# Kernel optimization log

Measured on AMD Instinct MI355X. Metric: run time of the kernel, lower is better.

## Reference

```python
import jax, jax.numpy as jnp
import numpy as np

B, L, H, D, M = 4, 2048, 16, 64, 128
EPS = 1e-6


def _create_projection_matrix(key, m, d):
    nb_full_blocks = m // d
    keys = jax.random.split(key, nb_full_blocks + 2)
    blocks = []
    for i in range(nb_full_blocks):
        unstructured = jax.random.normal(keys[i], (d, d), dtype=jnp.float32)
        q, _ = jnp.linalg.qr(unstructured)
        blocks.append(q.T)
    remaining = m - nb_full_blocks * d
    if remaining > 0:
        unstructured = jax.random.normal(keys[nb_full_blocks], (d, d), dtype=jnp.float32)
        q, _ = jnp.linalg.qr(unstructured)
        blocks.append(q.T[:remaining])
    final = jnp.concatenate(blocks, axis=0)  # [m, d]
    multiplier = jnp.linalg.norm(jax.random.normal(keys[-1], (m, d), dtype=jnp.float32), axis=1)
    return multiplier[:, None] * final


def setup_inputs() -> dict:
    key = jax.random.key(0)
    kq, kk, kv, kp = jax.random.split(key, 4)
    return {
        "q": jax.random.normal(kq, (B, L, H, D), dtype=jnp.float32),
        "k": jax.random.normal(kk, (B, L, H, D), dtype=jnp.float32),
        "v": jax.random.normal(kv, (B, L, H, D), dtype=jnp.float32),
        "projection_matrix": _create_projection_matrix(kp, M, D),
    }


def _softmax_kernel(data, proj, is_query, eps=EPS):
    # data: [B,L,H,D], proj: [M,D]
    data = (data.shape[-1] ** -0.25) * data
    ratio = proj.shape[0] ** -0.5
    data_dash = jnp.einsum('blhd,md->blhm', data, proj)  # [B,L,H,M]
    diag = jnp.sum(data * data, axis=-1, keepdims=True) * 0.5  # [B,L,H,1]
    if is_query:
        mx = jnp.max(data_dash, axis=-1, keepdims=True)
    else:
        mx = jnp.max(data_dash, axis=(1, 3), keepdims=True)
    return ratio * (jnp.exp(data_dash - diag - mx) + eps)


def reference(q, k, v, projection_matrix):
    qp = _softmax_kernel(q, projection_matrix, True)   # [B,L,H,M]
    kp = _softmax_kernel(k, projection_matrix, False)  # [B,L,H,M]
    # move L to the front for the causal scan
    qs = jnp.swapaxes(qp, 0, 1)  # [L,B,H,M]
    ks = jnp.swapaxes(kp, 0, 1)  # [L,B,H,M]
    vs = jnp.swapaxes(v, 0, 1)   # [L,B,H,D]

    def step(carry, inp):
        s, dsum = carry                 # s: [B,H,M,D], dsum: [B,H,M]
        q_t, k_t, v_t = inp
        s = s + k_t[..., :, None] * v_t[..., None, :]  # outer product accumulate
        dsum = dsum + k_t
        num = jnp.einsum('bhmd,bhm->bhd', s, q_t)      # [B,H,D]
        den = jnp.einsum('bhm,bhm->bh', q_t, dsum)     # [B,H]
        return (s, dsum), (num, den)

    init = (jnp.zeros((qs.shape[1], qs.shape[2], qs.shape[3], vs.shape[3]), qs.dtype),
            jnp.zeros_like(ks[0]))
    _, (nums, dens) = jax.lax.scan(step, init, (qs, ks, vs))
    av = jnp.swapaxes(nums, 0, 1)          # [B,L,H,D]
    norm = jnp.swapaxes(dens, 0, 1)[..., None]  # [B,L,H,1]
    return av / norm
```

## Files before the change

### kernel.cpp

```cpp
#include <hip/hip_runtime.h>
#include <math.h>

#define B_ 4
#define L_ 2048
#define H_ 16
#define D_ 64
#define M_ 128
#define TC_ 64
#define NC_ (L_ / TC_)
#define EPSK 1e-6f
#define DATA_SCALE 0.35355339059327379f
#define RATIO 0.08838834764831845f

typedef __bf16 bf16;
typedef bf16 bf16x4 __attribute__((ext_vector_type(4)));
typedef bf16 bf16x8 __attribute__((ext_vector_type(8)));
typedef float floatx4 __attribute__((ext_vector_type(4)));

#define PK128 136
#define PK64 72

__device__ __forceinline__ unsigned pk(bf16 a, bf16 b) {
    return (unsigned)__builtin_bit_cast(unsigned short, a) |
           ((unsigned)__builtin_bit_cast(unsigned short, b) << 16);
}

__device__ __forceinline__ unsigned enc_f(float f) {
    unsigned u = __float_as_uint(f);
    return (u & 0x80000000u) ? ~u : (u | 0x80000000u);
}
__device__ __forceinline__ float dec_f(unsigned u) {
    unsigned b = (u & 0x80000000u) ? (u ^ 0x80000000u) : ~u;
    return __uint_as_float(b);
}

__global__ __launch_bounds__(256) void proj_split(const float* __restrict__ proj,
                                                  bf16* __restrict__ pfh,
                                                  bf16* __restrict__ pfl,
                                                  unsigned* __restrict__ mx) {
    int f = blockIdx.x * 256 + threadIdx.x;
    if (blockIdx.x == 0 && threadIdx.x < B_ * H_) mx[threadIdx.x] = 0u;
    int tc = f >> 7, k0h = (f >> 6) & 1, lane = f & 63;
    int lr = lane & 15, quad = lane >> 4;
    const float* src = proj + (16 * tc + lr) * 64 + k0h * 32 + quad * 8;
    float4 x0 = *(const float4*)src;
    float4 x1 = *(const float4*)(src + 4);
    float a[8] = {x0.x, x0.y, x0.z, x0.w, x1.x, x1.y, x1.z, x1.w};
    bf16x8 hi, lo;
#pragma unroll
    for (int e = 0; e < 8; e++) {
        bf16 h = (bf16)a[e];
        hi[e] = h;
        lo[e] = (bf16)(a[e] - (float)h);
    }
    *(bf16x8*)(pfh + (size_t)f * 8) = hi;
    *(bf16x8*)(pfl + (size_t)f * 8) = lo;
}

template <int MODE>
__device__ __forceinline__ void feat_body(const float* __restrict__ data,
                                          const bf16* __restrict__ pfh,
                                          const bf16* __restrict__ pfl,
                                          unsigned* __restrict__ mxk,
                                          bf16* __restrict__ outp,
                                          bf16* __restrict__ outT,
                                          int blk, bf16* sc, float* wred) {
    int tid = threadIdx.x;
    int c = blk & 31, h = (blk >> 5) & 15, b = blk >> 9;
    int l0 = c * 64;
    int w = tid >> 6, lane = tid & 63, lr = lane & 15, quad = lane >> 4;

    const float* drow = data +
        ((size_t)(b * L_ + l0 + 16 * w + lr) * H_ + h) * D_ + quad * 8;
    bf16x8 ah[2], al[2];
    float ss = 0.f;
#pragma unroll
    for (int k0 = 0; k0 < 2; k0++) {
        float4 x0 = *(const float4*)(drow + k0 * 32);
        float4 x1 = *(const float4*)(drow + k0 * 32 + 4);
        float a[8] = {x0.x, x0.y, x0.z, x0.w, x1.x, x1.y, x1.z, x1.w};
#pragma unroll
        for (int e = 0; e < 8; e++) {
            float s = DATA_SCALE * a[e];
            if (MODE != 0) ss += s * s;
            bf16 hh = (bf16)s;
            ah[k0][e] = hh;
            if (MODE != 0) al[k0][e] = (bf16)(s - (float)hh);
        }
    }
    float ssrow = 0.f;
    if (MODE != 0) {
        ss += __shfl_xor(ss, 16, 64);
        ss += __shfl_xor(ss, 32, 64);
        ssrow = 0.5f * ss;
    }

    floatx4 acc[8];
#pragma unroll
    for (int tc = 0; tc < 8; tc++) acc[tc] = (floatx4){0.f, 0.f, 0.f, 0.f};

    const bf16x8* ph = (const bf16x8*)pfh + lane;
    const bf16x8* pl = (const bf16x8*)pfl + lane;
#pragma unroll
    for (int tc = 0; tc < 8; tc++) {
#pragma unroll
        for (int k0 = 0; k0 < 2; k0++) {
            bf16x8 bh = ph[(tc * 2 + k0) * 64];
            acc[tc] = __builtin_amdgcn_mfma_f32_16x16x32_bf16(ah[k0], bh, acc[tc], 0, 0, 0);
            if (MODE != 0) {
                bf16x8 bl = pl[(tc * 2 + k0) * 64];
                acc[tc] = __builtin_amdgcn_mfma_f32_16x16x32_bf16(al[k0], bh, acc[tc], 0, 0, 0);
                acc[tc] = __builtin_amdgcn_mfma_f32_16x16x32_bf16(ah[k0], bl, acc[tc], 0, 0, 0);
            }
        }
    }

    if (MODE == 0) {
        float mm = acc[0][0];
#pragma unroll
        for (int tc = 0; tc < 8; tc++)
#pragma unroll
            for (int reg = 0; reg < 4; reg++) mm = fmaxf(mm, acc[tc][reg]);
#pragma unroll
        for (int off = 1; off < 64; off <<= 1) mm = fmaxf(mm, __shfl_xor(mm, off, 64));
        if (lane == 0) wred[w] = mm;
        __syncthreads();
        if (tid == 0) {
            float g = fmaxf(fmaxf(wred[0], wred[1]), fmaxf(wred[2], wred[3]));
            atomicMax(&mxk[b * H_ + h], enc_f(g));
        }
        return;
    }

    int t0 = 16 * w + 4 * quad;
    float mxg = 0.f;
    if (MODE == 1) mxg = dec_f(mxk[b * H_ + h]);

    float rm[4];
    if (MODE == 2) {
#pragma unroll
        for (int reg = 0; reg < 4; reg++) {
            float m = acc[0][reg];
#pragma unroll
            for (int tc = 1; tc < 8; tc++) m = fmaxf(m, acc[tc][reg]);
            m = fmaxf(m, __shfl_xor(m, 1, 64));
            m = fmaxf(m, __shfl_xor(m, 2, 64));
            m = fmaxf(m, __shfl_xor(m, 4, 64));
            m = fmaxf(m, __shfl_xor(m, 8, 64));
            rm[reg] = m;
        }
    }

#pragma unroll
    for (int reg = 0; reg < 4; reg++) {
        float dg = __shfl(ssrow, 4 * quad + reg, 64);
        float sh = (MODE == 1) ? (dg + mxg) : (dg + rm[reg]);
#pragma unroll
        for (int tc = 0; tc < 8; tc++) {
            float val = RATIO * (__expf(acc[tc][reg] - sh) + EPSK);
            sc[(t0 + reg) * 130 + 16 * tc + lr] = (bf16)val;
        }
    }
    __syncthreads();

#pragma unroll
    for (int i = 0; i < 16; i++) {
        int e = tid + 256 * i;
        int row = e >> 6, mp = e & 63;
        unsigned u = pk(sc[row * 130 + 2 * mp], sc[row * 130 + 2 * mp + 1]);
        *(unsigned*)(outp + ((size_t)(b * L_ + l0 + row) * H_ + h) * M_ + 2 * mp) = u;
    }
    if (MODE == 1) {
#pragma unroll
        for (int i = 0; i < 16; i++) {
            int e = tid + 256 * i;
            int m = e >> 5, t2 = (e & 31) * 2;
            unsigned u = pk(sc[t2 * 130 + m], sc[(t2 + 1) * 130 + m]);
            *(unsigned*)(outT + ((size_t)(b * H_ + h) * M_ + m) * L_ + l0 + t2) = u;
        }
    }
}

__device__ __forceinline__ void vtr_body(const float* __restrict__ v,
                                         bf16* __restrict__ vbT,
                                         int blk, bf16* vt) {
    int tid = threadIdx.x;
    int c = blk & 31, hh = (blk >> 5) & 15, b = blk >> 9;
#pragma unroll
    for (int i = 0; i < 4; i++) {
        int ch = tid + 256 * i;
        int row = ch >> 4, c4 = ch & 15;
        size_t gb = ((size_t)(b * L_ + c * 64 + row) * H_ + hh) * D_;
        float4 x = *(const float4*)(v + gb + c4 * 4);
        unsigned* lp = (unsigned*)(vt + row * 66 + c4 * 4);
        lp[0] = pk((bf16)x.x, (bf16)x.y);
        lp[1] = pk((bf16)x.z, (bf16)x.w);
    }
    __syncthreads();
    size_t ob = (size_t)((b * H_ + hh) * D_) * (size_t)L_ + c * 64;
#pragma unroll
    for (int i = 0; i < 8; i++) {
        int e2 = tid + 256 * i;
        int d = e2 >> 5, tau2 = (e2 & 31) * 2;
        *(unsigned*)(vbT + ob + (size_t)d * L_ + tau2) =
            pk(vt[tau2 * 66 + d], vt[(tau2 + 1) * 66 + d]);
    }
}

__global__ __launch_bounds__(256) void pre3(const float* __restrict__ q,
                                            const float* __restrict__ k,
                                            const float* __restrict__ v,
                                            const bf16* __restrict__ pfh,
                                            const bf16* __restrict__ pfl,
                                            unsigned* __restrict__ mxk,
                                            bf16* __restrict__ qp,
                                            bf16* __restrict__ vbT) {
    __shared__ __align__(16) bf16 arena[64 * 130];
    __shared__ float wred[4];
    int blk = blockIdx.x;
    if (blk < 2048) {
        feat_body<2>(q, pfh, pfl, mxk, qp, (bf16*)nullptr, blk, arena, wred);
    } else if (blk < 4096) {
        feat_body<0>(k, pfh, pfl, mxk, (bf16*)nullptr, (bf16*)nullptr, blk - 2048,
                     arena, wred);
    } else {
        vtr_body(v, vbT, blk - 4096, arena);
    }
}

__global__ __launch_bounds__(256) void feat_k(const float* __restrict__ k,
                                              const bf16* __restrict__ pfh,
                                              const bf16* __restrict__ pfl,
                                              unsigned* __restrict__ mxk,
                                              bf16* __restrict__ kp,
                                              bf16* __restrict__ kpT) {
    __shared__ __align__(16) bf16 arena[64 * 130];
    __shared__ float wred[4];
    feat_body<1>(k, pfh, pfl, mxk, kp, kpT, blockIdx.x, arena, wred);
}

__global__ __launch_bounds__(256) void chunk_mfma(const bf16* __restrict__ kpT,
                                                  const bf16* __restrict__ vbT,
                                                  bf16* __restrict__ S,
                                                  float* __restrict__ ds) {
    __shared__ __align__(16) bf16 kT[128 * PK64];
    __shared__ __align__(16) bf16 vT[64 * PK64];
    int tid = threadIdx.x;
    int blk = blockIdx.x;
    int c = blk & 31, bh = blk >> 5;
    int l0 = c * 64;
#pragma unroll
    for (int i = 0; i < 4; i++) {
        int ch = tid + 256 * i;
        int m = ch >> 3, c8 = ch & 7;
        *(uint4*)(kT + m * PK64 + c8 * 8) =
            ((const uint4*)kpT)[(((size_t)bh * M_ + m) * L_ + l0) / 8 + c8];
    }
#pragma unroll
    for (int i = 0; i < 2; i++) {
        int ch = tid + 256 * i;
        int d = ch >> 3, c8 = ch & 7;
        *(uint4*)(vT + d * PK64 + c8 * 8) =
            ((const uint4*)vbT)[(((size_t)bh * D_ + d) * L_ + l0) / 8 + c8];
    }
    __syncthreads();

    int w = tid >> 6, lane = tid & 63, lr = lane & 15, quad = lane >> 4;
    floatx4 acc[8];
#pragma unroll
    for (int tc = 0; tc < 8; tc++) acc[tc] = (floatx4){0.f, 0.f, 0.f, 0.f};
#pragma unroll
    for (int k0 = 0; k0 < 64; k0 += 32) {
        bf16x8 a = *(const bf16x8*)(vT + (16 * w + lr) * PK64 + k0 + quad * 8);
#pragma unroll
        for (int tc = 0; tc < 8; tc++) {
            bf16x8 bb = *(const bf16x8*)(kT + (16 * tc + lr) * PK64 + k0 + quad * 8);
            acc[tc] = __builtin_amdgcn_mfma_f32_16x16x32_bf16(a, bb, acc[tc], 0, 0, 0);
        }
    }

    float dsv = 0.f;
    {
        int m = tid >> 1, half = tid & 1;
        const bf16x8* kr = (const bf16x8*)(kT + m * PK64 + half * 32);
#pragma unroll
        for (int j = 0; j < 4; j++) {
            bf16x8 vv = kr[j];
#pragma unroll
            for (int e = 0; e < 8; e++) dsv += (float)vv[e];
        }
        dsv += __shfl_xor(dsv, 1, 64);
    }
    __syncthreads();

    bf16* scr = kT;
    int d0 = 16 * w + 4 * quad;
#pragma unroll
    for (int tc = 0; tc < 8; tc++)
#pragma unroll
        for (int reg = 0; reg < 4; reg++)
            scr[(d0 + reg) * 128 + 16 * tc + lr] = (bf16)acc[tc][reg];
    if ((tid & 1) == 0) ds[(size_t)blk * M_ + (tid >> 1)] = dsv;
    __syncthreads();
#pragma unroll
    for (int i = 0; i < 4; i++) {
        int e = tid + 256 * i;
        ((uint4*)S)[(size_t)blk * 1024 + e] = ((const uint4*)scr)[e];
    }
}

__global__ void prefix_SD(unsigned* __restrict__ S, float* __restrict__ ds) {
    int blk = blockIdx.x;
    int seg = blk & 15, bh = blk >> 4;
    int p = seg * 256 + threadIdx.x;
    size_t base = (size_t)bh * NC_ * 4096 + p;
    unsigned uv[NC_];
#pragma unroll
    for (int c = 0; c < NC_; c++) uv[c] = S[base + (size_t)c * 4096];
    float c0 = 0.f, c1 = 0.f;
#pragma unroll
    for (int c = 0; c < NC_; c++) {
        unsigned u = uv[c];
        float f0 = (float)__builtin_bit_cast(bf16, (unsigned short)(u & 0xffffu));
        float f1 = (float)__builtin_bit_cast(bf16, (unsigned short)(u >> 16));
        S[base + (size_t)c * 4096] = pk((bf16)c0, (bf16)c1);
        c0 += f0; c1 += f1;
    }
    if (seg == 0 && threadIdx.x < 128) {
        int m = threadIdx.x;
        size_t dbase = (size_t)bh * NC_ * M_ + m;
        float dv[NC_];
#pragma unroll
        for (int c = 0; c < NC_; c++) dv[c] = ds[dbase + (size_t)c * M_];
        float carry = 0.f;
#pragma unroll
        for (int c = 0; c < NC_; c++) {
            ds[dbase + (size_t)c * M_] = carry;
            carry += dv[c];
        }
    }
}

__global__ __launch_bounds__(256, 4) void attn_mfma(const bf16* __restrict__ qp,
                                                    const bf16* __restrict__ kp,
                                                    const bf16* __restrict__ vbT,
                                                    const bf16* __restrict__ Sp,
                                                    const float* __restrict__ dp,
                                                    float* __restrict__ out) {
    __shared__ __align__(16) bf16 vT[64 * PK64];
    __shared__ __align__(16) bf16 sc[64 * PK64];
    __shared__ float dprevL[128];

    int tid = threadIdx.x;
    int blk = blockIdx.x;
    int c = blk & 31, bh = blk >> 5;
    int h = bh & 15, b = bh >> 4;
    int l0 = c * 64;
    int w = tid >> 6, lane = tid & 63, lr = lane & 15, quad = lane >> 4;

#pragma unroll
    for (int i = 0; i < 2; i++) {
        int ch = tid + 256 * i;
        int d = ch >> 3, c8 = ch & 7;
        *(uint4*)(vT + d * PK64 + c8 * 8) =
            ((const uint4*)vbT)[(((size_t)bh * D_ + d) * L_ + l0) / 8 + c8];
    }
    if (tid < 128) dprevL[tid] = dp[(size_t)blk * M_ + tid];

    bf16x8 af[4];
    {
        const bf16* qb = qp + ((size_t)(b * L_ + l0 + 16 * w + lr) * H_ + h) * M_ + quad * 8;
#pragma unroll
        for (int k = 0; k < 4; k++) af[k] = *(const bf16x8*)(qb + 32 * k);
    }
    __syncthreads();

    float den0v = 0.f;
#pragma unroll
    for (int k = 0; k < 4; k++)
#pragma unroll
        for (int e = 0; e < 8; e++)
            den0v += (float)af[k][e] * dprevL[quad * 8 + 32 * k + e];
    den0v += __shfl_xor(den0v, 16, 64);
    den0v += __shfl_xor(den0v, 32, 64);

    floatx4 acc[4];
#pragma unroll
    for (int tc = 0; tc < 4; tc++) acc[tc] = (floatx4){0.f, 0.f, 0.f, 0.f};

    {
        const bf16* spb = Sp + (size_t)blk * 8192;
#pragma unroll
        for (int ki = 0; ki < 4; ki++) {
#pragma unroll
            for (int tc = 0; tc < 4; tc++) {
                bf16x8 bb = *(const bf16x8*)(spb + (16 * tc + lr) * 128 + 32 * ki + quad * 8);
                acc[tc] = __builtin_amdgcn_mfma_f32_16x16x32_bf16(af[ki], bb, acc[tc], 0, 0, 0);
            }
        }
    }

    floatx4 acc2[4];
#pragma unroll
    for (int tc = 0; tc < 4; tc++) acc2[tc] = (floatx4){0.f, 0.f, 0.f, 0.f};
    {
        const bf16* kpb = kp + ((size_t)(b * L_ + l0) * H_ + h) * M_ + quad * 8;
#pragma unroll
        for (int ki = 0; ki < 4; ki++) {
            for (int tc = 0; tc <= w; tc++) {
                bf16x8 bb = *(const bf16x8*)(kpb + (size_t)(16 * tc + lr) * (H_ * M_) + 32 * ki);
                acc2[tc] = __builtin_amdgcn_mfma_f32_16x16x32_bf16(af[ki], bb, acc2[tc], 0, 0, 0);
            }
        }
    }

    int t0 = 16 * w + 4 * quad;
    float densc[4];
    {
        float dsum[4] = {0.f, 0.f, 0.f, 0.f};
#pragma unroll
        for (int tc = 0; tc < 4; tc++) {
#pragma unroll
            for (int reg = 0; reg < 4; reg++) {
                int tg = t0 + reg, tau = 16 * tc + lr;
                float vv = (tc <= w) ? acc2[tc][reg] : 0.f;
                if (tau > tg) vv = 0.f;
                dsum[reg] += vv;
                sc[tg * PK64 + tau] = (bf16)vv;
            }
        }
#pragma unroll
        for (int reg = 0; reg < 4; reg++) {
            float s = dsum[reg];
            s += __shfl_xor(s, 1, 64);
            s += __shfl_xor(s, 2, 64);
            s += __shfl_xor(s, 4, 64);
            s += __shfl_xor(s, 8, 64);
            densc[reg] = s;
        }
    }

    {
        int kmax = (w >= 2) ? 64 : 32;
        for (int k0 = 0; k0 < kmax; k0 += 32) {
            bf16x8 a = *(const bf16x8*)(sc + (16 * w + lr) * PK64 + k0 + quad * 8);
#pragma unroll
            for (int tc = 0; tc < 4; tc++) {
                bf16x8 bb = *(const bf16x8*)(vT + (16 * tc + lr) * PK64 + k0 + quad * 8);
                acc[tc] = __builtin_amdgcn_mfma_f32_16x16x32_bf16(a, bb, acc[tc], 0, 0, 0);
            }
        }
    }

    {
        float inv[4];
#pragma unroll
        for (int reg = 0; reg < 4; reg++) {
            float d0 = __shfl(den0v, 4 * quad + reg, 64);
            inv[reg] = 1.0f / (d0 + densc[reg]);
        }
#pragma unroll
        for (int tc = 0; tc < 4; tc++)
#pragma unroll
            for (int reg = 0; reg < 4; reg++)
                out[((size_t)(b * L_ + l0 + t0 + reg) * H_ + h) * D_ + 16 * tc + lr] =
                    acc[tc][reg] * inv[reg];
    }
}

extern "C" void kernel_launch(void* const* d_in, const int* in_sizes, int n_in,
                              void* d_out, int out_size, void* d_ws, size_t ws_size,
                              hipStream_t stream) {
    const float* q = (const float*)d_in[0];
    const float* k = (const float*)d_in[1];
    const float* v = (const float*)d_in[2];
    const float* proj = (const float*)d_in[3];
    float* out = (float*)d_out;
    char* W = (char*)d_ws;

    bf16* qp   = (bf16*)(W);
    bf16* kp   = (bf16*)(W + 33554432ull);
    bf16* kpT  = (bf16*)(W + 67108864ull);
    bf16* vbT  = (bf16*)(W + 100663296ull);
    bf16* S    = (bf16*)(W + 117440512ull);
    float* ds  = (float*)(W + 150994944ull);
    unsigned* mx = (unsigned*)(W + 152043520ull);
    bf16* pfh  = (bf16*)(W + 152043776ull);
    bf16* pfl  = (bf16*)(W + 152060160ull);

    hipLaunchKernelGGL(proj_split, dim3(4), dim3(256), 0, stream, proj, pfh, pfl, mx);
    hipLaunchKernelGGL(pre3, dim3(6144), dim3(256), 0, stream,
                       q, k, v, pfh, pfl, mx, qp, vbT);
    hipLaunchKernelGGL(feat_k, dim3(2048), dim3(256), 0, stream,
                       k, pfh, pfl, mx, kp, kpT);
    hipLaunchKernelGGL(chunk_mfma, dim3(2048), dim3(256), 0, stream, kpT, vbT, S, ds);
    hipLaunchKernelGGL(prefix_SD, dim3(1024), dim3(256), 0, stream, (unsigned*)S, ds);
    hipLaunchKernelGGL(attn_mfma, dim3(2048), dim3(256), 0, stream,
                       qp, kp, vbT, S, ds, out);
}
```

Baseline: 235.1 us.

## Fuse query feature map into attention kernel and drop transposed intermediates

Query features are now computed inside the attention kernel, so the bf16 qp buffer is never written or read back. The key max pass becomes its own kernel. Key features are stored chunk-contiguous and transposed in shared memory inside chunk_v, which replaces the separate kpT buffer. The V conversion and transpose also move into chunk_v. This cuts global memory traffic and the large workspace, but the attention kernel gets extra MFMA work, more registers and more shared memory, which may lower occupancy.

```diff
diff --git a/kernel.cpp b/kernel.cpp
--- a/kernel.cpp
+++ b/kernel.cpp
@@ -17,8 +17,8 @@
 typedef bf16 bf16x8 __attribute__((ext_vector_type(8)));
 typedef float floatx4 __attribute__((ext_vector_type(4)));
 
-#define PK128 136
 #define PK64 72
+#define FS_ 136
 
 __device__ __forceinline__ unsigned pk(bf16 a, bf16 b) {
     return (unsigned)__builtin_bit_cast(unsigned short, a) |
@@ -57,104 +57,111 @@
     *(bf16x8*)(pfl + (size_t)f * 8) = lo;
 }
 
-template <int MODE>
-__device__ __forceinline__ void feat_body(const float* __restrict__ data,
-                                          const bf16* __restrict__ pfh,
-                                          const bf16* __restrict__ pfl,
-                                          unsigned* __restrict__ mxk,
-                                          bf16* __restrict__ outp,
-                                          bf16* __restrict__ outT,
-                                          int blk, bf16* sc, float* wred) {
+__global__ __launch_bounds__(256) void feat_max(const float* __restrict__ k,
+                                                const bf16* __restrict__ pfh,
+                                                unsigned* __restrict__ mxk) {
+    __shared__ float wred[4];
     int tid = threadIdx.x;
+    int blk = blockIdx.x;
     int c = blk & 31, h = (blk >> 5) & 15, b = blk >> 9;
     int l0 = c * 64;
     int w = tid >> 6, lane = tid & 63, lr = lane & 15, quad = lane >> 4;
 
-    const float* drow = data +
+    const float* drow = k +
         ((size_t)(b * L_ + l0 + 16 * w + lr) * H_ + h) * D_ + quad * 8;
-    bf16x8 ah[2], al[2];
-    float ss = 0.f;
+    bf16x8 ah[2];
 #pragma unroll
     for (int k0 = 0; k0 < 2; k0++) {
         float4 x0 = *(const float4*)(drow + k0 * 32);
         float4 x1 = *(const float4*)(drow + k0 * 32 + 4);
         float a[8] = {x0.x, x0.y, x0.z, x0.w, x1.x, x1.y, x1.z, x1.w};
 #pragma unroll
-        for (int e = 0; e < 8; e++) {
-            float s = DATA_SCALE * a[e];
-            if (MODE != 0) ss += s * s;
-            bf16 hh = (bf16)s;
-            ah[k0][e] = hh;
-            if (MODE != 0) al[k0][e] = (bf16)(s - (float)hh);
-        }
-    }
-    float ssrow = 0.f;
-    if (MODE != 0) {
-        ss += __shfl_xor(ss, 16, 64);
-        ss += __shfl_xor(ss, 32, 64);
-        ssrow = 0.5f * ss;
+        for (int e = 0; e < 8; e++) ah[k0][e] = (bf16)(DATA_SCALE * a[e]);
     }
 
     floatx4 acc[8];
 #pragma unroll
     for (int tc = 0; tc < 8; tc++) acc[tc] = (floatx4){0.f, 0.f, 0.f, 0.f};
-
     const bf16x8* ph = (const bf16x8*)pfh + lane;
-    const bf16x8* pl = (const bf16x8*)pfl + lane;
-#pragma unroll
-    for (int tc = 0; tc < 8; tc++) {
+#pragma unroll
+    for (int tc = 0; tc < 8; tc++)
 #pragma unroll
         for (int k0 = 0; k0 < 2; k0++) {
             bf16x8 bh = ph[(tc * 2 + k0) * 64];
             acc[tc] = __builtin_amdgcn_mfma_f32_16x16x32_bf16(ah[k0], bh, acc[tc], 0, 0, 0);
-            if (MODE != 0) {
-                bf16x8 bl = pl[(tc * 2 + k0) * 64];
-                acc[tc] = __builtin_amdgcn_mfma_f32_16x16x32_bf16(al[k0], bh, acc[tc], 0, 0, 0);
-                acc[tc] = __builtin_amdgcn_mfma_f32_16x16x32_bf16(ah[k0], bl, acc[tc], 0, 0, 0);
-            }
-        }
-    }
-
-    if (MODE == 0) {
-        float mm = acc[0][0];
-#pragma unroll
-        for (int tc = 0; tc < 8; tc++)
-#pragma unroll
-            for (int reg = 0; reg < 4; reg++) mm = fmaxf(mm, acc[tc][reg]);
-#pragma unroll
-        for (int off = 1; off < 64; off <<= 1) mm = fmaxf(mm, __shfl_xor(mm, off, 64));
-        if (lane == 0) wred[w] = mm;
-        __syncthreads();
-        if (tid == 0) {
-            float g = fmaxf(fmaxf(wred[0], wred[1]), fmaxf(wred[2], wred[3]));
-            atomicMax(&mxk[b * H_ + h], enc_f(g));
-        }
-        return;
-    }
+        }
+
+    float mm = acc[0][0];
+#pragma unroll
+    for (int tc = 0; tc < 8; tc++)
+#pragma unroll
+        for (int reg = 0; reg < 4; reg++) mm = fmaxf(mm, acc[tc][reg]);
+#pragma unroll
+    for (int off = 1; off < 64; off <<= 1) mm = fmaxf(mm, __shfl_xor(mm, off, 64));
+    if (lane == 0) wred[w] = mm;
+    __syncthreads();
+    if (tid == 0) {
+        float g = fmaxf(fmaxf(wred[0], wred[1]), fmaxf(wred[2], wred[3]));
+        atomicMax(&mxk[b * H_ + h], enc_f(g));
+    }
+}
+
+__global__ __launch_bounds__(256) void feat_k(const float* __restrict__ kin,
+                                              const bf16* __restrict__ pfh,
+                                              const bf16* __restrict__ pfl,
+                                              const unsigned* __restrict__ mxk,
+                                              bf16* __restrict__ kp) {
+    __shared__ __align__(16) bf16 sc[64 * 130];
+    int tid = threadIdx.x;
+    int blk = blockIdx.x;
+    int c = blk & 31, h = (blk >> 5) & 15, b = blk >> 9;
+    int l0 = c * 64;
+    int w = tid >> 6, lane = tid & 63, lr = lane & 15, quad = lane >> 4;
+
+    const float* drow = kin +
+        ((size_t)(b * L_ + l0 + 16 * w + lr) * H_ + h) * D_ + quad * 8;
+    bf16x8 ah[2], al[2];
+    float ss = 0.f;
+#pragma unroll
+    for (int k0 = 0; k0 < 2; k0++) {
+        float4 x0 = *(const float4*)(drow + k0 * 32);
+        float4 x1 = *(const float4*)(drow + k0 * 32 + 4);
+        float a[8] = {x0.x, x0.y, x0.z, x0.w, x1.x, x1.y, x1.z, x1.w};
+#pragma unroll
+        for (int e = 0; e < 8; e++) {
+            float s = DATA_SCALE * a[e];
+            ss += s * s;
+            bf16 hh = (bf16)s;
+            ah[k0][e] = hh;
+            al[k0][e] = (bf16)(s - (float)hh);
+        }
+    }
+    ss += __shfl_xor(ss, 16, 64);
+    ss += __shfl_xor(ss, 32, 64);
+    float ssrow = 0.5f * ss;
+
+    floatx4 acc[8];
+#pragma unroll
+    for (int tc = 0; tc < 8; tc++) acc[tc] = (floatx4){0.f, 0.f, 0.f, 0.f};
+    const bf16x8* ph = (const bf16x8*)pfh + lane;
+    const bf16x8* pl = (const bf16x8*)pfl + lane;
+#pragma unroll
+    for (int tc = 0; tc < 8; tc++)
+#pragma unroll
+        for (int k0 = 0; k0 < 2; k0++) {
+            bf16x8 bh = ph[(tc * 2 + k0) * 64];
+            bf16x8 bl = pl[(tc * 2 + k0) * 64];
+            acc[tc] = __builtin_amdgcn_mfma_f32_16x16x32_bf16(ah[k0], bh, acc[tc], 0, 0, 0);
+            acc[tc] = __builtin_amdgcn_mfma_f32_16x16x32_bf16(al[k0], bh, acc[tc], 0, 0, 0);
+            acc[tc] = __builtin_amdgcn_mfma_f32_16x16x32_bf16(ah[k0], bl, acc[tc], 0, 0, 0);
+        }
 
     int t0 = 16 * w + 4 * quad;
-    float mxg = 0.f;
-    if (MODE == 1) mxg = dec_f(mxk[b * H_ + h]);
-
-    float rm[4];
-    if (MODE == 2) {
-#pragma unroll
-        for (int reg = 0; reg < 4; reg++) {
-            float m = acc[0][reg];
-#pragma unroll
-            for (int tc = 1; tc < 8; tc++) m = fmaxf(m, acc[tc][reg]);
-            m = fmaxf(m, __shfl_xor(m, 1, 64));
-            m = fmaxf(m, __shfl_xor(m, 2, 64));
-            m = fmaxf(m, __shfl_xor(m, 4, 64));
-            m = fmaxf(m, __shfl_xor(m, 8, 64));
-            rm[reg] = m;
-        }
-    }
-
+    float mxg = dec_f(mxk[b * H_ + h]);
 #pragma unroll
     for (int reg = 0; reg < 4; reg++) {
         float dg = __shfl(ssrow, 4 * quad + reg, 64);
-        float sh = (MODE == 1) ? (dg + mxg) : (dg + rm[reg]);
+        float sh = dg + mxg;
 #pragma unroll
         for (int tc = 0; tc < 8; tc++) {
             float val = RATIO * (__expf(acc[tc][reg] - sh) + EPSK);
@@ -163,109 +170,52 @@
     }
     __syncthreads();
 
+    bf16* kout = kp + (size_t)blk * 8192;
 #pragma unroll
     for (int i = 0; i < 16; i++) {
         int e = tid + 256 * i;
         int row = e >> 6, mp = e & 63;
-        unsigned u = pk(sc[row * 130 + 2 * mp], sc[row * 130 + 2 * mp + 1]);
-        *(unsigned*)(outp + ((size_t)(b * L_ + l0 + row) * H_ + h) * M_ + 2 * mp) = u;
-    }
-    if (MODE == 1) {
-#pragma unroll
-        for (int i = 0; i < 16; i++) {
-            int e = tid + 256 * i;
-            int m = e >> 5, t2 = (e & 31) * 2;
-            unsigned u = pk(sc[t2 * 130 + m], sc[(t2 + 1) * 130 + m]);
-            *(unsigned*)(outT + ((size_t)(b * H_ + h) * M_ + m) * L_ + l0 + t2) = u;
-        }
-    }
-}
-
-__device__ __forceinline__ void vtr_body(const float* __restrict__ v,
-                                         bf16* __restrict__ vbT,
-                                         int blk, bf16* vt) {
-    int tid = threadIdx.x;
-    int c = blk & 31, hh = (blk >> 5) & 15, b = blk >> 9;
-#pragma unroll
-    for (int i = 0; i < 4; i++) {
-        int ch = tid + 256 * i;
-        int row = ch >> 4, c4 = ch & 15;
-        size_t gb = ((size_t)(b * L_ + c * 64 + row) * H_ + hh) * D_;
-        float4 x = *(const float4*)(v + gb + c4 * 4);
-        unsigned* lp = (unsigned*)(vt + row * 66 + c4 * 4);
-        lp[0] = pk((bf16)x.x, (bf16)x.y);
-        lp[1] = pk((bf16)x.z, (bf16)x.w);
-    }
-    __syncthreads();
-    size_t ob = (size_t)((b * H_ + hh) * D_) * (size_t)L_ + c * 64;
-#pragma unroll
-    for (int i = 0; i < 8; i++) {
-        int e2 = tid + 256 * i;
-        int d = e2 >> 5, tau2 = (e2 & 31) * 2;
-        *(unsigned*)(vbT + ob + (size_t)d * L_ + tau2) =
-            pk(vt[tau2 * 66 + d], vt[(tau2 + 1) * 66 + d]);
-    }
-}
-
-__global__ __launch_bounds__(256) void pre3(const float* __restrict__ q,
-                                            const float* __restrict__ k,
-                                            const float* __restrict__ v,
-                                            const bf16* __restrict__ pfh,
-                                            const bf16* __restrict__ pfl,
-                                            unsigned* __restrict__ mxk,
-                                            bf16* __restrict__ qp,
-                                            bf16* __restrict__ vbT) {
-    __shared__ __align__(16) bf16 arena[64 * 130];
-    __shared__ float wred[4];
-    int blk = blockIdx.x;
-    if (blk < 2048) {
-        feat_body<2>(q, pfh, pfl, mxk, qp, (bf16*)nullptr, blk, arena, wred);
-    } else if (blk < 4096) {
-        feat_body<0>(k, pfh, pfl, mxk, (bf16*)nullptr, (bf16*)nullptr, blk - 2048,
-                     arena, wred);
-    } else {
-        vtr_body(v, vbT, blk - 4096, arena);
-    }
-}
-
-__global__ __launch_bounds__(256) void feat_k(const float* __restrict__ k,
-                                              const bf16* __restrict__ pfh,
-                                              const bf16* __restrict__ pfl,
-                                              unsigned* __restrict__ mxk,
-                                              bf16* __restrict__ kp,
-                                              bf16* __restrict__ kpT) {
-    __shared__ __align__(16) bf16 arena[64 * 130];
-    __shared__ float wred[4];
-    feat_body<1>(k, pfh, pfl, mxk, kp, kpT, blockIdx.x, arena, wred);
-}
-
-__global__ __launch_bounds__(256) void chunk_mfma(const bf16* __restrict__ kpT,
-                                                  const bf16* __restrict__ vbT,
-                                                  bf16* __restrict__ S,
-                                                  float* __restrict__ ds) {
+        *(unsigned*)(kout + row * 128 + 2 * mp) =
+            pk(sc[row * 130 + 2 * mp], sc[row * 130 + 2 * mp + 1]);
+    }
+}
+
+__global__ __launch_bounds__(256) void chunk_v(const bf16* __restrict__ kp,
+                                               const float* __restrict__ v,
+                                               bf16* __restrict__ S,
+                                               float* __restrict__ ds,
+                                               bf16* __restrict__ vbT) {
     __shared__ __align__(16) bf16 kT[128 * PK64];
     __shared__ __align__(16) bf16 vT[64 * PK64];
     int tid = threadIdx.x;
     int blk = blockIdx.x;
     int c = blk & 31, bh = blk >> 5;
+    int h = bh & 15, b = bh >> 4;
     int l0 = c * 64;
+    int w = tid >> 6, lane = tid & 63, lr = lane & 15, quad = lane >> 4;
+
+    const bf16* kpt = kp + (size_t)blk * 8192;
 #pragma unroll
     for (int i = 0; i < 4; i++) {
-        int ch = tid + 256 * i;
-        int m = ch >> 3, c8 = ch & 7;
-        *(uint4*)(kT + m * PK64 + c8 * 8) =
-            ((const uint4*)kpT)[(((size_t)bh * M_ + m) * L_ + l0) / 8 + c8];
-    }
-#pragma unroll
-    for (int i = 0; i < 2; i++) {
-        int ch = tid + 256 * i;
-        int d = ch >> 3, c8 = ch & 7;
-        *(uint4*)(vT + d * PK64 + c8 * 8) =
-            ((const uint4*)vbT)[(((size_t)bh * D_ + d) * L_ + l0) / 8 + c8];
-    }
-    __syncthreads();
-
-    int w = tid >> 6, lane = tid & 63, lr = lane & 15, quad = lane >> 4;
+        int m8 = w * 4 + i;
+        bf16x8 kv = *(const bf16x8*)(kpt + lane * 128 + m8 * 8);
+#pragma unroll
+        for (int e = 0; e < 8; e++) kT[(m8 * 8 + e) * PK64 + lane] = kv[e];
+    }
+    {
+        const float* vrow = v + ((size_t)(b * L_ + l0 + lane) * H_ + h) * D_;
+#pragma unroll
+        for (int i = 0; i < 4; i++) {
+            int d4 = w * 4 + i;
+            float4 x = *(const float4*)(vrow + d4 * 4);
+            vT[(d4 * 4 + 0) * PK64 + lane] = (bf16)x.x;
+            vT[(d4 * 4 + 1) * PK64 + lane] = (bf16)x.y;
+            vT[(d4 * 4 + 2) * PK64 + lane] = (bf16)x.z;
+            vT[(d4 * 4 + 3) * PK64 + lane] = (bf16)x.w;
+        }
+    }
+    __syncthreads();
+
     floatx4 acc[8];
 #pragma unroll
     for (int tc = 0; tc < 8; tc++) acc[tc] = (floatx4){0.f, 0.f, 0.f, 0.f};
@@ -276,6 +226,17 @@
         for (int tc = 0; tc < 8; tc++) {
             bf16x8 bb = *(const bf16x8*)(kT + (16 * tc + lr) * PK64 + k0 + quad * 8);
             acc[tc] = __builtin_amdgcn_mfma_f32_16x16x32_bf16(a, bb, acc[tc], 0, 0, 0);
+        }
+    }
+
+    {
+        size_t ob = (size_t)(bh * D_) * (size_t)L_ + l0;
+#pragma unroll
+        for (int i = 0; i < 8; i++) {
+            int e2 = tid + 256 * i;
+            int d = e2 >> 5, tau2 = (e2 & 31) * 2;
+            *(unsigned*)(vbT + ob + (size_t)d * L_ + tau2) =
+                *(const unsigned*)(vT + d * PK64 + tau2);
         }
     }
 
@@ -341,15 +302,18 @@
     }
 }
 
-__global__ __launch_bounds__(256, 4) void attn_mfma(const bf16* __restrict__ qp,
-                                                    const bf16* __restrict__ kp,
-                                                    const bf16* __restrict__ vbT,
-                                                    const bf16* __restrict__ Sp,
-                                                    const float* __restrict__ dp,
-                                                    float* __restrict__ out) {
+__global__ __launch_bounds__(256, 4) void attn_q(const float* __restrict__ q,
+                                                 const bf16* __restrict__ pfh,
+                                                 const bf16* __restrict__ pfl,
+                                                 const bf16* __restrict__ kp,
+                                                 const bf16* __restrict__ vbT,
+                                                 const bf16* __restrict__ Sp,
+                                                 const float* __restrict__ dp,
+                                                 float* __restrict__ out) {
+    __shared__ __align__(16) bf16 fsc[64 * FS_];
     __shared__ __align__(16) bf16 vT[64 * PK64];
-    __shared__ __align__(16) bf16 sc[64 * PK64];
     __shared__ float dprevL[128];
+    bf16* sc = fsc;
 
     int tid = threadIdx.x;
     int blk = blockIdx.x;
@@ -367,13 +331,69 @@
     }
     if (tid < 128) dprevL[tid] = dp[(size_t)blk * M_ + tid];
 
+    const float* drow = q +
+        ((size_t)(b * L_ + l0 + 16 * w + lr) * H_ + h) * D_ + quad * 8;
+    bf16x8 ah[2], al[2];
+    float ss = 0.f;
+#pragma unroll
+    for (int k0 = 0; k0 < 2; k0++) {
+        float4 x0 = *(const float4*)(drow + k0 * 32);
+        float4 x1 = *(const float4*)(drow + k0 * 32 + 4);
+        float a[8] = {x0.x, x0.y, x0.z, x0.w, x1.x, x1.y, x1.z, x1.w};
+#pragma unroll
+        for (int e = 0; e < 8; e++) {
+            float s = DATA_SCALE * a[e];
+            ss += s * s;
+            bf16 hh = (bf16)s;
+            ah[k0][e] = hh;
+            al[k0][e] = (bf16)(s - (float)hh);
+        }
+    }
+    ss += __shfl_xor(ss, 16, 64);
+    ss += __shfl_xor(ss, 32, 64);
+    float ssrow = 0.5f * ss;
+
+    floatx4 facc[8];
+#pragma unroll
+    for (int tc = 0; tc < 8; tc++) facc[tc] = (floatx4){0.f, 0.f, 0.f, 0.f};
+    {
+        const bf16x8* ph = (const bf16x8*)pfh + lane;
+        const bf16x8* pl = (const bf16x8*)pfl + lane;
+#pragma unroll
+        for (int tc = 0; tc < 8; tc++)
+#pragma unroll
+            for (int k0 = 0; k0 < 2; k0++) {
+                bf16x8 bh = ph[(tc * 2 + k0) * 64];
+                bf16x8 bl = pl[(tc * 2 + k0) * 64];
+                facc[tc] = __builtin_amdgcn_mfma_f32_16x16x32_bf16(ah[k0], bh, facc[tc], 0, 0, 0);
+                facc[tc] = __builtin_amdgcn_mfma_f32_16x16x32_bf16(al[k0], bh, facc[tc], 0, 0, 0);
+                facc[tc] = __builtin_amdgcn_mfma_f32_16x16x32_bf16(ah[k0], bl, facc[tc], 0, 0, 0);
+            }
+    }
+    int t0 = 16 * w + 4 * quad;
+#pragma unroll
+    for (int reg = 0; reg < 4; reg++) {
+        float m = facc[0][reg];
+#pragma unroll
+        for (int tc = 1; tc < 8; tc++) m = fmaxf(m, facc[tc][reg]);
+        m = fmaxf(m, __shfl_xor(m, 1, 64));
+        m = fmaxf(m, __shfl_xor(m, 2, 64));
+        m = fmaxf(m, __shfl_xor(m, 4, 64));
+        m = fmaxf(m, __shfl_xor(m, 8, 64));
+        float dg = __shfl(ssrow, 4 * quad + reg, 64);
+        float sh = dg + m;
+#pragma unroll
+        for (int tc = 0; tc < 8; tc++) {
+            float val = RATIO * (__expf(facc[tc][reg] - sh) + EPSK);
+            fsc[(t0 + reg) * FS_ + 16 * tc + lr] = (bf16)val;
+        }
+    }
+    __syncthreads();
+
     bf16x8 af[4];
-    {
-        const bf16* qb = qp + ((size_t)(b * L_ + l0 + 16 * w + lr) * H_ + h) * M_ + quad * 8;
-#pragma unroll
-        for (int k = 0; k < 4; k++) af[k] = *(const bf16x8*)(qb + 32 * k);
-    }
-    __syncthreads();
+#pragma unroll
+    for (int k = 0; k < 4; k++)
+        af[k] = *(const bf16x8*)(fsc + (16 * w + lr) * FS_ + 32 * k + quad * 8);
 
     float den0v = 0.f;
 #pragma unroll
@@ -404,17 +424,17 @@
 #pragma unroll
     for (int tc = 0; tc < 4; tc++) acc2[tc] = (floatx4){0.f, 0.f, 0.f, 0.f};
     {
-        const bf16* kpb = kp + ((size_t)(b * L_ + l0) * H_ + h) * M_ + quad * 8;
+        const bf16* kpb = kp + (size_t)blk * 8192 + quad * 8;
 #pragma unroll
         for (int ki = 0; ki < 4; ki++) {
             for (int tc = 0; tc <= w; tc++) {
-                bf16x8 bb = *(const bf16x8*)(kpb + (size_t)(16 * tc + lr) * (H_ * M_) + 32 * ki);
+                bf16x8 bb = *(const bf16x8*)(kpb + (16 * tc + lr) * 128 + 32 * ki);
                 acc2[tc] = __builtin_amdgcn_mfma_f32_16x16x32_bf16(af[ki], bb, acc2[tc], 0, 0, 0);
             }
         }
     }
-
-    int t0 = 16 * w + 4 * quad;
+    __syncthreads();
+
     float densc[4];
     {
         float dsum[4] = {0.f, 0.f, 0.f, 0.f};
@@ -478,23 +498,19 @@
     float* out = (float*)d_out;
     char* W = (char*)d_ws;
 
-    bf16* qp   = (bf16*)(W);
-    bf16* kp   = (bf16*)(W + 33554432ull);
-    bf16* kpT  = (bf16*)(W + 67108864ull);
-    bf16* vbT  = (bf16*)(W + 100663296ull);
-    bf16* S    = (bf16*)(W + 117440512ull);
-    float* ds  = (float*)(W + 150994944ull);
-    unsigned* mx = (unsigned*)(W + 152043520ull);
-    bf16* pfh  = (bf16*)(W + 152043776ull);
-    bf16* pfl  = (bf16*)(W + 152060160ull);
+    bf16* kp   = (bf16*)(W);
+    bf16* vbT  = (bf16*)(W + 33554432ull);
+    bf16* S    = (bf16*)(W + 50331648ull);
+    float* ds  = (float*)(W + 83886080ull);
+    unsigned* mx = (unsigned*)(W + 84934656ull);
+    bf16* pfh  = (bf16*)(W + 84934912ull);
+    bf16* pfl  = (bf16*)(W + 84951296ull);
 
     hipLaunchKernelGGL(proj_split, dim3(4), dim3(256), 0, stream, proj, pfh, pfl, mx);
-    hipLaunchKernelGGL(pre3, dim3(6144), dim3(256), 0, stream,
-                       q, k, v, pfh, pfl, mx, qp, vbT);
-    hipLaunchKernelGGL(feat_k, dim3(2048), dim3(256), 0, stream,
-                       k, pfh, pfl, mx, kp, kpT);
-    hipLaunchKernelGGL(chunk_mfma, dim3(2048), dim3(256), 0, stream, kpT, vbT, S, ds);
+    hipLaunchKernelGGL(feat_max, dim3(2048), dim3(256), 0, stream, k, pfh, mx);
+    hipLaunchKernelGGL(feat_k, dim3(2048), dim3(256), 0, stream, k, pfh, pfl, mx, kp);
+    hipLaunchKernelGGL(chunk_v, dim3(2048), dim3(256), 0, stream, kp, v, S, ds, vbT);
     hipLaunchKernelGGL(prefix_SD, dim3(1024), dim3(256), 0, stream, (unsigned*)S, ds);
-    hipLaunchKernelGGL(attn_mfma, dim3(2048), dim3(256), 0, stream,
-                       qp, kp, vbT, S, ds, out);
-}
+    hipLaunchKernelGGL(attn_q, dim3(2048), dim3(256), 0, stream,
+                       q, pfh, pfl, kp, vbT, S, ds, out);
+}
```

New measurement: 236.5 us. About the same (+0.6%).
